# Kernel tuning notes

Measured on AMD Instinct MI355X. Metric: run time of the kernel, lower is better.

The kernel has to match this reference:

```python
import jax, jax.numpy as jnp
import numpy as np
from jax import lax

C = 768
SHIFT_DISTANCES = (1, 2, 3)


def _layernorm(x, g, b, eps=1e-5):
    m = jnp.mean(x, axis=-1, keepdims=True)
    v = jnp.mean((x - m) ** 2, axis=-1, keepdims=True)
    return (x - m) * lax.rsqrt(v + eps) * g + b


def setup_inputs() -> dict:
    key = jax.random.key(0)
    ks = jax.random.split(key, 16)
    B, T, N = 8, 16, 197
    inp = {
        "x": jax.random.normal(ks[0], (B * T, N, C), dtype=jnp.float32),
        "ln_g": jnp.ones((C,), jnp.float32),
        "ln_b": jnp.zeros((C,), jnp.float32),
        "gate_w": jax.random.normal(ks[1], (C, C), jnp.float32) * 0.02,
        "gate_b": jnp.zeros((C,), jnp.float32),
        "proj_w1": jax.random.normal(ks[2], (C, C), jnp.float32) * 0.02,
        "proj_b1": jnp.zeros((C,), jnp.float32),
        "proj_w2": jax.random.normal(ks[3], (C, C), jnp.float32) * 0.02,
        "proj_b2": jnp.zeros((C,), jnp.float32),
        "fusion_w": jnp.ones((len(SHIFT_DISTANCES),), jnp.float32),
        "num_frames": T,
    }
    for i, d in enumerate(SHIFT_DISTANCES):
        k = 2 * d + 1
        # depthwise Conv1d weight: (out=C, in/groups=1, k)
        inp[f"conv_w{i}"] = jax.random.normal(ks[4 + i], (C, 1, k), jnp.float32) * (1.0 / np.sqrt(k))
        inp[f"conv_b{i}"] = jnp.zeros((C,), jnp.float32)
    return inp


def _branch(x4, conv_w, conv_b, d, ln_g, ln_b, gate_w, gate_b):
    # x4: [B, T, N, C]
    B, T, N, Cc = x4.shape
    p = Cc // 3  # past / future split; static gets the remainder
    x_norm = jax.nn.relu(_layernorm(x4, ln_g, ln_b))
    # [B, T, N, C] -> [B*N, C, T] for depthwise conv over time
    x_1d = x_norm.transpose(0, 2, 3, 1).reshape(B * N, Cc, T)
    feat = lax.conv_general_dilated(
        x_1d, conv_w, window_strides=(1,), padding=[(d, d)],
        dimension_numbers=("NCH", "OIH", "NCH"), feature_group_count=Cc,
    ) + conv_b[None, :, None]
    feat = feat.reshape(B, N, Cc, T).transpose(0, 3, 1, 2)  # [B, T, N, C]
    gate = jax.nn.sigmoid(jnp.einsum("btnc,cd->btnd", feat, gate_w) + gate_b)
    y = gate * x4  # channelwise split-and-multiply fuses into one op
    y_past, y_future, y_static = y[..., :p], y[..., p:2 * p], y[..., 2 * p:]
    s = min(d, T)
    out_past = jnp.pad(y_past[:, s:], ((0, 0), (0, s), (0, 0), (0, 0)))  # lshift
    out_future = jnp.pad(y_future[:, :T - s], ((0, 0), (s, 0), (0, 0), (0, 0)))  # rshift
    return jnp.concatenate([out_past, out_future, y_static], axis=-1)


def reference(x, ln_g, ln_b, gate_w, gate_b, proj_w1, proj_b1, proj_w2, proj_b2,
              fusion_w, conv_w0, conv_b0, conv_w1, conv_b1, conv_w2, conv_b2,
              num_frames):
    B_T, N, Cc = x.shape
    T = num_frames
    B = B_T // T
    x4 = x.reshape(B, T, N, Cc)
    convs = [(conv_w0, conv_b0), (conv_w1, conv_b1), (conv_w2, conv_b2)]
    outs = jnp.stack([
        _branch(x4, cw, cb, d, ln_g, ln_b, gate_w, gate_b)
        for (cw, cb), d in zip(convs, SHIFT_DISTANCES)
    ], axis=0)  # [3, B, T, N, C]
    w = jax.nn.softmax(fusion_w)[:, None, None, None, None]
    fused = jnp.sum(w * outs, axis=0).reshape(B_T, N, Cc)
    h = jnp.einsum("bnc,cd->bnd", fused, proj_w1) + proj_b1
    h = jax.nn.gelu(h, approximate=False)
    h = jnp.einsum("bnc,cd->bnd", h, proj_w2) + proj_b2
    return x + h
```

## Files before the change

### kernel.cpp

```cpp
#include <hip/hip_runtime.h>
#include <math.h>


#define MROWS 25216
#define CD    768
#define NTOK  197
#define TFR   16

typedef __attribute__((ext_vector_type(8))) short short8;
typedef __attribute__((ext_vector_type(4))) float floatx4;
typedef unsigned int u32;

__device__ __forceinline__ unsigned short f2bf(float f) {
    union { float f; unsigned u; } v; v.f = f;
    unsigned r = v.u + 0x7FFFu + ((v.u >> 16) & 1u);
    return (unsigned short)(r >> 16);
}
__device__ __forceinline__ float bf2f(unsigned short h) {
    union { unsigned u; float f; } v; v.u = ((unsigned)h) << 16;
    return v.f;
}

__device__ __forceinline__ void gl2lds16(const void* g, void* l) {
    __builtin_amdgcn_global_load_lds(
        (__attribute__((address_space(1))) void*)(unsigned long long)g,
        (__attribute__((address_space(3))) void*)(u32)(unsigned long long)l,
        16, 0, 0);
}

__global__ __launch_bounds__(256)
void ln_relu_kernel(const float* __restrict__ x, const float* __restrict__ g,
                    const float* __restrict__ b, unsigned short* __restrict__ xn,
                    unsigned short* __restrict__ xb) {
    int row = blockIdx.x;
    int tid = threadIdx.x;
    const float* xr = x + (size_t)row * CD;
    float v0 = xr[tid], v1 = xr[tid + 256], v2 = xr[tid + 512];
    float s = v0 + v1 + v2;
    __shared__ float red[8];
#pragma unroll
    for (int off = 32; off; off >>= 1) s += __shfl_down(s, off, 64);
    int lane = tid & 63, w = tid >> 6;
    if (lane == 0) red[w] = s;
    __syncthreads();
    float mean = (red[0] + red[1] + red[2] + red[3]) * (1.0f / CD);
    float d0 = v0 - mean, d1 = v1 - mean, d2 = v2 - mean;
    float s2 = d0 * d0 + d1 * d1 + d2 * d2;
#pragma unroll
    for (int off = 32; off; off >>= 1) s2 += __shfl_down(s2, off, 64);
    if (lane == 0) red[4 + w] = s2;
    __syncthreads();
    float var = (red[4] + red[5] + red[6] + red[7]) * (1.0f / CD);
    float inv = rsqrtf(var + 1e-5f);
    unsigned short* xo = xn + (size_t)row * CD;
    unsigned short* xc = xb + (size_t)row * CD;
    float o0 = fmaxf(d0 * inv * g[tid]       + b[tid],       0.0f);
    float o1 = fmaxf(d1 * inv * g[tid + 256] + b[tid + 256], 0.0f);
    float o2 = fmaxf(d2 * inv * g[tid + 512] + b[tid + 512], 0.0f);
    xo[tid] = f2bf(o0); xo[tid + 256] = f2bf(o1); xo[tid + 512] = f2bf(o2);
    xc[tid] = f2bf(v0); xc[tid + 256] = f2bf(v1); xc[tid + 512] = f2bf(v2);
}

template <int D>
__global__ __launch_bounds__(256)
void dwconv_kernel(const unsigned short* __restrict__ xn, const float* __restrict__ cw,
                   const float* __restrict__ cb, unsigned short* __restrict__ feat) {
    constexpr int KK = 2 * D + 1;
    int gid = blockIdx.x * 256 + threadIdx.x;
    int bn = gid / 96;
    int cg = gid - bn * 96;
    int c0 = cg * 8;
    int b = bn / NTOK;
    size_t base = ((size_t)b * TFR * NTOK + (bn - b * NTOK)) * CD + c0;
    const size_t tstride = (size_t)NTOK * CD;

    short8 u[TFR];
#pragma unroll
    for (int t = 0; t < TFR; ++t)
        u[t] = *(const short8*)(xn + base + (size_t)t * tstride);

    float wgt[8][KK], bb[8];
#pragma unroll
    for (int q = 0; q < 8; ++q) {
        bb[q] = cb[c0 + q];
#pragma unroll
        for (int j = 0; j < KK; ++j) wgt[q][j] = cw[(c0 + q) * KK + j];
    }

#pragma unroll
    for (int t = 0; t < TFR; ++t) {
        float acc[8];
#pragma unroll
        for (int q = 0; q < 8; ++q) acc[q] = bb[q];
#pragma unroll
        for (int j = 0; j < KK; ++j) {
            int tj = t + j - D;
            if (tj < 0 || tj >= TFR) continue;
#pragma unroll
            for (int q = 0; q < 8; ++q)
                acc[q] += bf2f((unsigned short)u[tj][q]) * wgt[q][j];
        }
        short8 o;
#pragma unroll
        for (int q = 0; q < 8; ++q) o[q] = (short)f2bf(acc[q]);
        *(short8*)(feat + base + (size_t)t * tstride) = o;
    }
}

__global__ __launch_bounds__(256)
void wprep3_kernel(const float* __restrict__ w0, const float* __restrict__ w1,
                   const float* __restrict__ w2, unsigned short* __restrict__ t0,
                   unsigned short* __restrict__ t1, unsigned short* __restrict__ t2) {
    const float* w = blockIdx.y == 0 ? w0 : blockIdx.y == 1 ? w1 : w2;
    unsigned short* wt = blockIdx.y == 0 ? t0 : blockIdx.y == 1 ? t1 : t2;
    int gid = blockIdx.x * 256 + threadIdx.x;
    int n = gid / CD, k = gid - n * CD;
    wt[gid] = f2bf(w[(size_t)k * CD + n]);
}

__global__ __launch_bounds__(256)
void fuse_kernel(const unsigned short* __restrict__ y1,
                 const unsigned short* __restrict__ y2,
                 const unsigned short* __restrict__ y3,
                 unsigned short* __restrict__ fused) {
    int gid = blockIdx.x * 256 + threadIdx.x;
    int m = gid / 96;
    int kk = (gid - m * 96) * 8;
    int t = (m / NTOK) & 15;
    float vals[8] = {0.f, 0.f, 0.f, 0.f, 0.f, 0.f, 0.f, 0.f};
    const unsigned short* ys[3] = {y1, y2, y3};
#pragma unroll
    for (int d = 1; d <= 3; ++d) {
        int src; bool ok;
        if (kk < 256)      { src = m + d * NTOK; ok = (t + d) < TFR; }
        else if (kk < 512) { src = m - d * NTOK; ok = (t - d) >= 0; }
        else               { src = m;            ok = true; }
        if (ok) {
            short8 u = *(const short8*)(ys[d - 1] + (size_t)src * CD + kk);
#pragma unroll
            for (int e = 0; e < 8; ++e) vals[e] += bf2f((unsigned short)u[e]);
        }
    }
    short8 o;
#pragma unroll
    for (int e = 0; e < 8; ++e) o[e] = (short)f2bf(vals[e]);
    *(short8*)(fused + (size_t)m * CD + kk) = o;
}

template <int EPI>
__global__ __launch_bounds__(256)
void gemm_kernel(const unsigned short* __restrict__ A,
                 const unsigned short* __restrict__ Bt,
                 const float* __restrict__ bias,
                 const unsigned short* __restrict__ xb,
                 const float* __restrict__ xf,
                 float* __restrict__ outf,
                 unsigned short* __restrict__ outh,
                 const float* __restrict__ fw,
                 int widx) {
    __shared__ unsigned short As[4][128 * 32];
    __shared__ unsigned short Bs[4][128 * 32];
    int tid  = threadIdx.x;
    int m0   = blockIdx.x * 128;
    int n0   = blockIdx.y * 128;
    int wave = tid >> 6, lane = tid & 63;
    int wm   = (wave >> 1) * 64, wn = (wave & 1) * 64;
    int quad = lane >> 4, l16 = lane & 15;
    int r4   = lane >> 2;
    int ckx  = (((lane & 3) ^ ((lane >> 3) & 3)) * 8);
    int rdsl = (quad ^ ((l16 >> 1) & 3)) * 8;

    const size_t arow = (size_t)(m0 + wave * 16 + r4) * CD + ckx;
    const size_t brow = (size_t)(n0 + wave * 16 + r4) * CD + ckx;
    const size_t skip = (size_t)64 * CD;

    floatx4 acc[4][4];
#pragma unroll
    for (int i = 0; i < 4; ++i)
#pragma unroll
        for (int j = 0; j < 4; ++j) acc[i][j] = (floatx4){0.f, 0.f, 0.f, 0.f};

    auto stage = [&](int t, int b) {
        const size_t ko = (size_t)t * 32;
#pragma unroll
        for (int h = 0; h < 2; ++h) {
            gl2lds16(A  + arow + h * skip + ko, &As[b][(wave + h * 4) * 512]);
            gl2lds16(Bt + brow + h * skip + ko, &Bs[b][(wave + h * 4) * 512]);
        }
    };
    auto compute = [&](int b) {
        short8 af[4], bfr[4];
#pragma unroll
        for (int i = 0; i < 4; ++i) af[i]  = *(const short8*)(&As[b][(wm + i * 16 + l16) * 32 + rdsl]);
#pragma unroll
        for (int j = 0; j < 4; ++j) bfr[j] = *(const short8*)(&Bs[b][(wn + j * 16 + l16) * 32 + rdsl]);
#pragma unroll
        for (int i = 0; i < 4; ++i)
#pragma unroll
            for (int j = 0; j < 4; ++j)
                acc[i][j] = __builtin_amdgcn_mfma_f32_16x16x32_bf16(af[i], bfr[j], acc[i][j], 0, 0, 0);
    };

    constexpr int NT = CD / 32;
    stage(0, 0);
    stage(1, 1);
    stage(2, 2);
    for (int t = 0; t < NT - 2; ++t) {
        asm volatile("s_waitcnt vmcnt(8)" ::: "memory");
        __builtin_amdgcn_s_barrier();
        __builtin_amdgcn_sched_barrier(0);
        if (t + 3 < NT) stage(t + 3, (t + 3) & 3);
        compute(t & 3);
    }
    asm volatile("s_waitcnt vmcnt(4)" ::: "memory");
    __builtin_amdgcn_s_barrier();
    __builtin_amdgcn_sched_barrier(0);
    compute((NT - 2) & 3);
    asm volatile("s_waitcnt vmcnt(0)" ::: "memory");
    __builtin_amdgcn_s_barrier();
    __builtin_amdgcn_sched_barrier(0);
    compute((NT - 1) & 3);

    float wd = 0.f;
    if (EPI == 0) {
        float f0 = fw[0], f1 = fw[1], f2 = fw[2];
        float mx = fmaxf(f0, fmaxf(f1, f2));
        float e0 = expf(f0 - mx), e1 = expf(f1 - mx), e2 = expf(f2 - mx);
        float inv = 1.f / (e0 + e1 + e2);
        wd = (widx == 0 ? e0 : widx == 1 ? e1 : e2) * inv;
    }

#pragma unroll
    for (int j = 0; j < 4; ++j) {
        int col = n0 + wn + j * 16 + l16;
        float bc = bias[col];
#pragma unroll
        for (int i = 0; i < 4; ++i) {
#pragma unroll
            for (int r = 0; r < 4; ++r) {
                int row = m0 + wm + i * 16 + quad * 4 + r;
                size_t idx = (size_t)row * CD + col;
                float v = acc[i][j][r] + bc;
                if (EPI == 0) {
                    float gte = 1.f / (1.f + expf(-v));
                    outh[idx] = f2bf(wd * gte * bf2f(xb[idx]));
                } else if (EPI == 1) {
                    float gl = 0.5f * v * (1.0f + erff(v * 0.70710678118f));
                    outh[idx] = f2bf(gl);
                } else {
                    outf[idx] = v + xf[idx];
                }
            }
        }
    }
}

extern "C" void kernel_launch(void* const* d_in, const int* in_sizes, int n_in,
                              void* d_out, int out_size, void* d_ws, size_t ws_size,
                              hipStream_t stream) {
    const float* x      = (const float*)d_in[0];
    const float* ln_g   = (const float*)d_in[1];
    const float* ln_b   = (const float*)d_in[2];
    const float* gate_w = (const float*)d_in[3];
    const float* gate_b = (const float*)d_in[4];
    const float* pw1    = (const float*)d_in[5];
    const float* pb1    = (const float*)d_in[6];
    const float* pw2    = (const float*)d_in[7];
    const float* pb2    = (const float*)d_in[8];
    const float* fw     = (const float*)d_in[9];
    const float* cw[3]  = {(const float*)d_in[11], (const float*)d_in[13], (const float*)d_in[15]};
    const float* cb[3]  = {(const float*)d_in[12], (const float*)d_in[14], (const float*)d_in[16]};

    char* ws = (char*)d_ws;
    const size_t SB = (size_t)MROWS * CD * 2;
    unsigned short* gwt  = (unsigned short*)(ws + 0);
    unsigned short* p1t  = (unsigned short*)(ws + 1179648);
    unsigned short* p2t  = (unsigned short*)(ws + 2359296);
    unsigned short* xn   = (unsigned short*)(ws + 3538944);
    unsigned short* xb   = (unsigned short*)(ws + 3538944 + SB);
    unsigned short* feat = (unsigned short*)(ws + 3538944 + 2 * SB);
    unsigned short* y1   = (unsigned short*)(ws + 3538944 + 3 * SB);
    unsigned short* y2   = (unsigned short*)(ws + 3538944 + 4 * SB);
    unsigned short* y3   = (unsigned short*)(ws + 3538944 + 5 * SB);
    unsigned short* fused = feat;
    unsigned short* h1    = y1;

    dim3 wg(2304, 3);
    wprep3_kernel<<<wg, 256, 0, stream>>>(gate_w, pw1, pw2, gwt, p1t, p2t);
    ln_relu_kernel<<<MROWS, 256, 0, stream>>>(x, ln_g, ln_b, xn, xb);

    dim3 gg(197, 6);
    dwconv_kernel<1><<<591, 256, 0, stream>>>(xn, cw[0], cb[0], feat);
    gemm_kernel<0><<<gg, 256, 0, stream>>>(feat, gwt, gate_b, xb, nullptr,
                                           nullptr, y1, fw, 0);
    dwconv_kernel<2><<<591, 256, 0, stream>>>(xn, cw[1], cb[1], feat);
    gemm_kernel<0><<<gg, 256, 0, stream>>>(feat, gwt, gate_b, xb, nullptr,
                                           nullptr, y2, fw, 1);
    dwconv_kernel<3><<<591, 256, 0, stream>>>(xn, cw[2], cb[2], feat);
    gemm_kernel<0><<<gg, 256, 0, stream>>>(feat, gwt, gate_b, xb, nullptr,
                                           nullptr, y3, fw, 2);

    fuse_kernel<<<9456, 256, 0, stream>>>(y1, y2, y3, fused);

    gemm_kernel<1><<<gg, 256, 0, stream>>>(fused, p1t, pb1, nullptr, nullptr,
                                           nullptr, h1, nullptr, 0);
    gemm_kernel<2><<<gg, 256, 0, stream>>>(h1, p2t, pb2, nullptr, x,
                                           (float*)d_out, nullptr, nullptr, 0);
}
```

Before: 591.3 us.

## Stage GEMM epilogue through LDS for vectorized stores; merge depthwise convs into one launch

The GEMM epilogue now writes accumulators into shared memory, which reuses the operand staging buffers, in two halves. It then reads them back so each thread issues 16-byte coalesced loads and stores of the bias/sigmoid-gate, GELU or residual outputs, instead of scattered 2- or 4-byte accesses. The three depthwise conv launches are merged into one kernel with a 3-deep grid writing three separate feature buffers, and workspace aliasing is reshuffled so this fits. The cost is extra LDS round trips and barriers in the epilogue, plus more live workspace buffers.

```diff
diff --git a/kernel.cpp b/kernel.cpp
--- a/kernel.cpp
+++ b/kernel.cpp
@@ -62,9 +62,9 @@
 }
 
 template <int D>
-__global__ __launch_bounds__(256)
-void dwconv_kernel(const unsigned short* __restrict__ xn, const float* __restrict__ cw,
-                   const float* __restrict__ cb, unsigned short* __restrict__ feat) {
+__device__ __forceinline__
+void dw_body(const unsigned short* __restrict__ xn, const float* __restrict__ cw,
+             const float* __restrict__ cb, unsigned short* __restrict__ feat) {
     constexpr int KK = 2 * D + 1;
     int gid = blockIdx.x * 256 + threadIdx.x;
     int bn = gid / 96;
@@ -105,6 +105,18 @@
         for (int q = 0; q < 8; ++q) o[q] = (short)f2bf(acc[q]);
         *(short8*)(feat + base + (size_t)t * tstride) = o;
     }
+}
+
+__global__ __launch_bounds__(256)
+void dwconv_all(const unsigned short* __restrict__ xn,
+                const float* __restrict__ cw0, const float* __restrict__ cb0,
+                const float* __restrict__ cw1, const float* __restrict__ cb1,
+                const float* __restrict__ cw2, const float* __restrict__ cb2,
+                unsigned short* __restrict__ f1, unsigned short* __restrict__ f2,
+                unsigned short* __restrict__ f3) {
+    if (blockIdx.y == 0)      dw_body<1>(xn, cw0, cb0, f1);
+    else if (blockIdx.y == 1) dw_body<2>(xn, cw1, cb1, f2);
+    else                      dw_body<3>(xn, cw2, cb2, f3);
 }
 
 __global__ __launch_bounds__(256)
@@ -158,8 +170,11 @@
                  unsigned short* __restrict__ outh,
                  const float* __restrict__ fw,
                  int widx) {
-    __shared__ unsigned short As[4][128 * 32];
-    __shared__ unsigned short Bs[4][128 * 32];
+    __shared__ __align__(16) char smem[65536];
+    unsigned short (*As)[128 * 32] = (unsigned short (*)[128 * 32])smem;
+    unsigned short (*Bs)[128 * 32] = (unsigned short (*)[128 * 32])(smem + 32768);
+    float (*fE)[132] = (float (*)[132])smem;
+
     int tid  = threadIdx.x;
     int m0   = blockIdx.x * 128;
     int n0   = blockIdx.y * 128;
@@ -231,25 +246,56 @@
     }
 
 #pragma unroll
-    for (int j = 0; j < 4; ++j) {
-        int col = n0 + wn + j * 16 + l16;
-        float bc = bias[col];
-#pragma unroll
-        for (int i = 0; i < 4; ++i) {
-#pragma unroll
-            for (int r = 0; r < 4; ++r) {
-                int row = m0 + wm + i * 16 + quad * 4 + r;
-                size_t idx = (size_t)row * CD + col;
-                float v = acc[i][j][r] + bc;
-                if (EPI == 0) {
-                    float gte = 1.f / (1.f + expf(-v));
-                    outh[idx] = f2bf(wd * gte * bf2f(xb[idx]));
-                } else if (EPI == 1) {
-                    float gl = 0.5f * v * (1.0f + erff(v * 0.70710678118f));
-                    outh[idx] = f2bf(gl);
-                } else {
-                    outf[idx] = v + xf[idx];
+    for (int p = 0; p < 2; ++p) {
+        __syncthreads();
+        if (wm == p * 64) {
+#pragma unroll
+            for (int j = 0; j < 4; ++j) {
+                int col = wn + j * 16 + l16;
+                float bc = bias[n0 + col];
+#pragma unroll
+                for (int i = 0; i < 4; ++i)
+#pragma unroll
+                    for (int r = 0; r < 4; ++r)
+                        fE[i * 16 + quad * 4 + r][col] = acc[i][j][r] + bc;
+            }
+        }
+        __syncthreads();
+#pragma unroll
+        for (int it = 0; it < 4; ++it) {
+            int lr   = it * 16 + (tid >> 4);
+            int cg   = tid & 15;
+            size_t grow = (size_t)(m0 + p * 64 + lr);
+            int gcol = n0 + cg * 8;
+            size_t idx = grow * CD + gcol;
+            floatx4 v0 = *(const floatx4*)&fE[lr][cg * 8];
+            floatx4 v1 = *(const floatx4*)&fE[lr][cg * 8 + 4];
+            if (EPI == 0) {
+                short8 xv = *(const short8*)(xb + idx);
+                short8 o;
+#pragma unroll
+                for (int e = 0; e < 8; ++e) {
+                    float vv = e < 4 ? v0[e] : v1[e - 4];
+                    float gte = 1.f / (1.f + expf(-vv));
+                    o[e] = (short)f2bf(wd * gte * bf2f((unsigned short)xv[e]));
                 }
+                *(short8*)(outh + idx) = o;
+            } else if (EPI == 1) {
+                short8 o;
+#pragma unroll
+                for (int e = 0; e < 8; ++e) {
+                    float vv = e < 4 ? v0[e] : v1[e - 4];
+                    float gl = 0.5f * vv * (1.0f + erff(vv * 0.70710678118f));
+                    o[e] = (short)f2bf(gl);
+                }
+                *(short8*)(outh + idx) = o;
+            } else {
+                floatx4 x0 = *(const floatx4*)(xf + idx);
+                floatx4 x1 = *(const floatx4*)(xf + idx + 4);
+#pragma unroll
+                for (int e = 0; e < 4; ++e) { v0[e] += x0[e]; v1[e] += x1[e]; }
+                *(floatx4*)(outf + idx)     = v0;
+                *(floatx4*)(outf + idx + 4) = v1;
             }
         }
     }
@@ -278,26 +324,29 @@
     unsigned short* p2t  = (unsigned short*)(ws + 2359296);
     unsigned short* xn   = (unsigned short*)(ws + 3538944);
     unsigned short* xb   = (unsigned short*)(ws + 3538944 + SB);
-    unsigned short* feat = (unsigned short*)(ws + 3538944 + 2 * SB);
-    unsigned short* y1   = (unsigned short*)(ws + 3538944 + 3 * SB);
-    unsigned short* y2   = (unsigned short*)(ws + 3538944 + 4 * SB);
-    unsigned short* y3   = (unsigned short*)(ws + 3538944 + 5 * SB);
-    unsigned short* fused = feat;
-    unsigned short* h1    = y1;
+    unsigned short* f1   = (unsigned short*)(ws + 3538944 + 2 * SB);
+    unsigned short* f2   = (unsigned short*)(ws + 3538944 + 3 * SB);
+    unsigned short* f3   = (unsigned short*)(ws + 3538944 + 4 * SB);
+    unsigned short* y1    = xn;
+    unsigned short* y2    = f1;
+    unsigned short* y3    = f2;
+    unsigned short* fused = f3;
+    unsigned short* h1    = xn;
 
     dim3 wg(2304, 3);
     wprep3_kernel<<<wg, 256, 0, stream>>>(gate_w, pw1, pw2, gwt, p1t, p2t);
     ln_relu_kernel<<<MROWS, 256, 0, stream>>>(x, ln_g, ln_b, xn, xb);
 
+    dim3 dg(591, 3);
+    dwconv_all<<<dg, 256, 0, stream>>>(xn, cw[0], cb[0], cw[1], cb[1], cw[2], cb[2],
+                                       f1, f2, f3);
+
     dim3 gg(197, 6);
-    dwconv_kernel<1><<<591, 256, 0, stream>>>(xn, cw[0], cb[0], feat);
-    gemm_kernel<0><<<gg, 256, 0, stream>>>(feat, gwt, gate_b, xb, nullptr,
+    gemm_kernel<0><<<gg, 256, 0, stream>>>(f1, gwt, gate_b, xb, nullptr,
                                            nullptr, y1, fw, 0);
-    dwconv_kernel<2><<<591, 256, 0, stream>>>(xn, cw[1], cb[1], feat);
-    gemm_kernel<0><<<gg, 256, 0, stream>>>(feat, gwt, gate_b, xb, nullptr,
+    gemm_kernel<0><<<gg, 256, 0, stream>>>(f2, gwt, gate_b, xb, nullptr,
                                            nullptr, y2, fw, 1);
-    dwconv_kernel<3><<<591, 256, 0, stream>>>(xn, cw[2], cb[2], feat);
-    gemm_kernel<0><<<gg, 256, 0, stream>>>(feat, gwt, gate_b, xb, nullptr,
+    gemm_kernel<0><<<gg, 256, 0, stream>>>(f3, gwt, gate_b, xb, nullptr,
                                            nullptr, y3, fw, 2);
 
     fuse_kernel<<<9456, 256, 0, stream>>>(y1, y2, y3, fused);
```

Result: faster. 554.9 us (-6.2%).
